# Kernel optimization log

Measured on AMD Instinct MI355X. Metric: run time of the kernel, lower is better.

## Reference

```python
import math
import jax, jax.numpy as jnp
import numpy as np

THETA_RES = 1.0
RHO_RES = 1.0


def _hough_index_table(H, W, theta_res=THETA_RES, rho_res=RHO_RES):
    """Precomputed rho-bin index per (angle, pixel), as in the C_dht CUDA kernel."""
    numangle = int(math.ceil(180.0 / theta_res))
    D = math.sqrt((H - 1) ** 2 + (W - 1) ** 2)
    numrho = int(math.ceil(2.0 * D / rho_res) + 1)
    thetas = np.arange(numangle) * (np.pi / numangle)          # [A]
    xs = (np.arange(W) - W // 2).astype(np.float64)            # centered cols
    ys = (np.arange(H) - H // 2).astype(np.float64)            # centered rows
    # rho[a, y, x] = (x*cos(theta_a) + y*sin(theta_a)) / rho_res
    rho = (xs[None, None, :] * np.cos(thetas)[:, None, None]
           + ys[None, :, None] * np.sin(thetas)[:, None, None]) / rho_res
    ridx = np.round(rho).astype(np.int32) + numrho // 2
    ridx = np.clip(ridx, 0, numrho - 1)
    return jnp.asarray(ridx.reshape(numangle, H * W)), numangle, numrho


def setup_inputs() -> dict:
    key = jax.random.key(0)
    feat = jax.random.normal(key, (4, 128, 256, 256), dtype=jnp.float32)
    return {"feat": feat}


def reference(feat):
    N, C, H, W = feat.shape
    ridx, numangle, numrho = _hough_index_table(H, W)
    # pixels-major layout so segment_sum scatters over the leading axis
    x = feat.reshape(N * C, H * W).T                            # [P, N*C]
    scatter = lambda idx: jax.ops.segment_sum(x, idx, num_segments=numrho)
    acc = jax.vmap(scatter)(ridx)                               # [A, numrho, N*C]
    return acc.transpose(2, 0, 1).reshape(N, C, numangle, numrho)
```

## Files before the change

### kernel.cpp

```cpp
#include <hip/hip_runtime.h>
#include <hip/hip_fp16.h>
#include <cmath>


#define NA 180
#define NR 723
#define HW 65536
#define NC 512
#define ROW_W 368
#define ROW_PAD 368
#define RBASE 176
#define NWIN 32

__device__ __forceinline__ bool is_phase2(int a) { return a >= 46 && a <= 134; }

struct __align__(8) h4 { __half2 a, b; };

__global__ __launch_bounds__(256) void dht_win(unsigned int* __restrict__ win) {
    const int lane = threadIdx.x;
    const int w = blockIdx.x;
    const int a = blockIdx.y;
    const double theta = (double)a * (M_PI / 180.0);
    const double c = cos(theta), s = sin(theta);
    const bool p2 = is_phase2(a);
    int prev = 0;
    unsigned int word = 0;
    #pragma unroll
    for (int i = 0; i < 8; ++i) {
        const int k = w * 8 + i;
        const int x = p2 ? k : lane;
        const int y = p2 ? lane : k;
        const double rho = __dadd_rn(__dmul_rn((double)(x - 128), c),
                                     __dmul_rn((double)(y - 128), s));
        int r = (int)rint(rho) + 361;
        r = min(max(r, 0), NR - 1);
        if (i == 0) word = (unsigned int)r;
        else if (r != prev) word |= (1u << (15 + i));
        prev = r;
    }
    win[((size_t)a * NWIN + w) * 256 + lane] = word;
}

__global__ __launch_bounds__(256) void zero_out(float4* __restrict__ o, int n4) {
    const int i = blockIdx.x * 256 + threadIdx.x;
    if (i < n4) o[i] = make_float4(0.f, 0.f, 0.f, 0.f);
}

template <int SGN>
__device__ __forceinline__ void walk_one(const uint4 wq,
                                         const __half2 (&pxA)[8][4],
                                         const __half2 (&pxB)[8][4],
                                         h4* __restrict__ rp) {
    #pragma unroll
    for (int j = 0; j < 4; ++j) {
        const unsigned int wrd = (&wq.x)[j];
        int bin = (int)(wrd & 0xffffu) - RBASE;
        #pragma unroll
        for (int k = 0; k < 8; ++k) {
            if (k) bin += SGN * (int)((wrd >> (15 + k)) & 1u);
            h4 v = rp[bin];
            v.a = __hadd2(v.a, pxA[k][j]);
            v.b = __hadd2(v.b, pxB[k][j]);
            rp[bin] = v;
        }
    }
}

template <int SGN0, int SGN1>
__device__ __forceinline__ void walk_dual(const uint4 wq0, const uint4 wq1,
                                          const __half2 (&pxA)[8][4],
                                          const __half2 (&pxB)[8][4],
                                          h4* __restrict__ rpA,
                                          h4* __restrict__ rpB) {
    #pragma unroll
    for (int j = 0; j < 4; ++j) {
        const unsigned int w0 = (&wq0.x)[j];
        const unsigned int w1 = (&wq1.x)[j];
        int b0 = (int)(w0 & 0xffffu) - RBASE;
        int b1 = (int)(w1 & 0xffffu) - RBASE;
        #pragma unroll
        for (int k = 0; k < 8; ++k) {
            if (k) {
                b0 += SGN0 * (int)((w0 >> (15 + k)) & 1u);
                b1 += SGN1 * (int)((w1 >> (15 + k)) & 1u);
            }
            h4 vA = rpA[b0];
            h4 vB = rpB[b1];
            vA.a = __hadd2(vA.a, pxA[k][j]);
            vA.b = __hadd2(vA.b, pxB[k][j]);
            vB.a = __hadd2(vB.a, pxA[k][j]);
            vB.b = __hadd2(vB.b, pxB[k][j]);
            rpA[b0] = vA;
            rpB[b1] = vB;
        }
    }
}

__global__ __launch_bounds__(1024, 4) void dht_main(const float* __restrict__ feat,
                                                    const unsigned int* __restrict__ win,
                                                    float* __restrict__ out) {
    __shared__ h4 rowsA[16 * ROW_PAD];
    __shared__ h4 rowsB[16 * ROW_PAD];
    const int t = threadIdx.x;
    const int wv = t >> 6;
    const int l = t & 63;
    const int quad = blockIdx.x;
    const int phase = blockIdx.y;
    const int h = blockIdx.z;
    const int w = 16 * h + wv;
    const int k0 = 8 * w;
    const float* __restrict__ f0 = feat + (size_t)(4 * quad + 0) * HW;
    const float* __restrict__ f1 = feat + (size_t)(4 * quad + 1) * HW;
    const float* __restrict__ f2 = feat + (size_t)(4 * quad + 2) * HW;
    const float* __restrict__ f3 = feat + (size_t)(4 * quad + 3) * HW;
    float* __restrict__ o0 = out + (size_t)(4 * quad + 0) * (NA * NR);
    float* __restrict__ o1 = out + (size_t)(4 * quad + 1) * (NA * NR);
    float* __restrict__ o2 = out + (size_t)(4 * quad + 2) * (NA * NR);
    float* __restrict__ o3 = out + (size_t)(4 * quad + 3) * (NA * NR);

    const int fj0 = 2 * l;
    const int fj2 = 2 * l + 128;

    __half2 pxA[8][4], pxB[8][4];
    if (phase == 0) {
        #pragma unroll
        for (int k = 0; k < 8; ++k) {
            const int ro = (k0 + k) << 8;
            const float2 v0a = *(const float2*)(f0 + ro + fj0);
            const float2 v1a = *(const float2*)(f1 + ro + fj0);
            const float2 v2a = *(const float2*)(f2 + ro + fj0);
            const float2 v3a = *(const float2*)(f3 + ro + fj0);
            const float2 v0b = *(const float2*)(f0 + ro + fj2);
            const float2 v1b = *(const float2*)(f1 + ro + fj2);
            const float2 v2b = *(const float2*)(f2 + ro + fj2);
            const float2 v3b = *(const float2*)(f3 + ro + fj2);
            pxA[k][0] = __floats2half2_rn(v0a.x, v1a.x);
            pxB[k][0] = __floats2half2_rn(v2a.x, v3a.x);
            pxA[k][1] = __floats2half2_rn(v0a.y, v1a.y);
            pxB[k][1] = __floats2half2_rn(v2a.y, v3a.y);
            pxA[k][2] = __floats2half2_rn(v0b.x, v1b.x);
            pxB[k][2] = __floats2half2_rn(v2b.x, v3b.x);
            pxA[k][3] = __floats2half2_rn(v0b.y, v1b.y);
            pxB[k][3] = __floats2half2_rn(v2b.y, v3b.y);
        }
    } else {
        #pragma unroll
        for (int j = 0; j < 4; ++j) {
            const int fr = (j < 2) ? (fj0 + j) : (fj2 + (j - 2));
            const int ro = fr << 8;
            const float4 q0 = *(const float4*)(f0 + ro + k0);
            const float4 q1 = *(const float4*)(f0 + ro + k0 + 4);
            const float4 r0 = *(const float4*)(f1 + ro + k0);
            const float4 r1 = *(const float4*)(f1 + ro + k0 + 4);
            const float4 s0 = *(const float4*)(f2 + ro + k0);
            const float4 s1 = *(const float4*)(f2 + ro + k0 + 4);
            const float4 t0 = *(const float4*)(f3 + ro + k0);
            const float4 t1 = *(const float4*)(f3 + ro + k0 + 4);
            pxA[0][j] = __floats2half2_rn(q0.x, r0.x);
            pxB[0][j] = __floats2half2_rn(s0.x, t0.x);
            pxA[1][j] = __floats2half2_rn(q0.y, r0.y);
            pxB[1][j] = __floats2half2_rn(s0.y, t0.y);
            pxA[2][j] = __floats2half2_rn(q0.z, r0.z);
            pxB[2][j] = __floats2half2_rn(s0.z, t0.z);
            pxA[3][j] = __floats2half2_rn(q0.w, r0.w);
            pxB[3][j] = __floats2half2_rn(s0.w, t0.w);
            pxA[4][j] = __floats2half2_rn(q1.x, r1.x);
            pxB[4][j] = __floats2half2_rn(s1.x, t1.x);
            pxA[5][j] = __floats2half2_rn(q1.y, r1.y);
            pxB[5][j] = __floats2half2_rn(s1.y, t1.y);
            pxA[6][j] = __floats2half2_rn(q1.z, r1.z);
            pxB[6][j] = __floats2half2_rn(s1.z, t1.z);
            pxA[7][j] = __floats2half2_rn(q1.w, r1.w);
            pxB[7][j] = __floats2half2_rn(s1.w, t1.w);
        }
    }

    const int nAng = phase ? 89 : 91;
    for (int cb = 0; cb < nAng; cb += 2) {
        const int cn = min(2, nAng - cb);
        {
            float2* zA = (float2*)rowsA;
            float2* zB = (float2*)rowsB;
            for (int i = t; i < 16 * ROW_PAD; i += 1024) {
                zA[i] = make_float2(0.f, 0.f);
                zB[i] = make_float2(0.f, 0.f);
            }
        }
        __syncthreads();

        const int a0 = phase ? (46 + cb) : (cb <= 45 ? cb : cb + 89);
        h4* __restrict__ rpA = rowsA + wv * ROW_PAD;
        if (cn == 2) {
            const int ax1 = cb + 1;
            const int a1 = phase ? (46 + ax1) : (ax1 <= 45 ? ax1 : ax1 + 89);
            const unsigned int* wr0 = win + ((size_t)a0 * NWIN + w) * 256;
            const unsigned int* wr1 = win + ((size_t)a1 * NWIN + w) * 256;
            const uint2 p00 = *(const uint2*)(wr0 + fj0);
            const uint2 p01 = *(const uint2*)(wr0 + fj2);
            const uint2 p10 = *(const uint2*)(wr1 + fj0);
            const uint2 p11 = *(const uint2*)(wr1 + fj2);
            uint4 wq0; wq0.x = p00.x; wq0.y = p00.y; wq0.z = p01.x; wq0.w = p01.y;
            uint4 wq1; wq1.x = p10.x; wq1.y = p10.y; wq1.z = p11.x; wq1.w = p11.y;
            h4* __restrict__ rpB = rowsB + wv * ROW_PAD;
            if (!phase || a1 <= 90)
                walk_dual<+1, +1>(wq0, wq1, pxA, pxB, rpA, rpB);
            else if (a0 > 90)
                walk_dual<-1, -1>(wq0, wq1, pxA, pxB, rpA, rpB);
            else
                walk_dual<+1, -1>(wq0, wq1, pxA, pxB, rpA, rpB);
        } else {
            const unsigned int* wr0 = win + ((size_t)a0 * NWIN + w) * 256;
            const uint2 p00 = *(const uint2*)(wr0 + fj0);
            const uint2 p01 = *(const uint2*)(wr0 + fj2);
            uint4 wq0; wq0.x = p00.x; wq0.y = p00.y; wq0.z = p01.x; wq0.w = p01.y;
            if (phase && a0 > 90) walk_one<-1>(wq0, pxA, pxB, rpA);
            else                  walk_one<+1>(wq0, pxA, pxB, rpA);
        }
        __syncthreads();

        for (int i = t; i < cn * ROW_W; i += 1024) {
            const int al = i / ROW_W;
            const int rl = i - al * ROW_W;
            const h4* __restrict__ src = al ? rowsB : rowsA;
            float s0 = 0.f, s1 = 0.f, s2 = 0.f, s3 = 0.f;
            #pragma unroll
            for (int c2 = 0; c2 < 16; ++c2) {
                const h4 v = src[c2 * ROW_PAD + rl];
                s0 += __low2float(v.a); s1 += __high2float(v.a);
                s2 += __low2float(v.b); s3 += __high2float(v.b);
            }
            const int aidx = cb + al;
            const int a = phase ? (46 + aidx) : (aidx <= 45 ? aidx : aidx + 89);
            const size_t o = (size_t)a * NR + (RBASE + rl);
            unsafeAtomicAdd(o0 + o, s0);
            unsafeAtomicAdd(o1 + o, s1);
            unsafeAtomicAdd(o2 + o, s2);
            unsafeAtomicAdd(o3 + o, s3);
        }
        __syncthreads();
    }
}

extern "C" void kernel_launch(void* const* d_in, const int* in_sizes, int n_in,
                              void* d_out, int out_size, void* d_ws, size_t ws_size,
                              hipStream_t stream) {
    const float* feat = (const float*)d_in[0];
    float* out = (float*)d_out;
    unsigned int* win = (unsigned int*)d_ws;

    const size_t win_bytes = (size_t)NA * NWIN * 256 * sizeof(unsigned int);
    if (ws_size < win_bytes) return;

    const int n4 = out_size / 4;
    hipLaunchKernelGGL(zero_out, dim3((n4 + 255) / 256), dim3(256), 0, stream,
                       (float4*)out, n4);
    hipLaunchKernelGGL(dht_win, dim3(NWIN, NA), dim3(256), 0, stream, win);
    hipLaunchKernelGGL(dht_main, dim3(NC / 4, 2, 2), dim3(1024), 0, stream,
                       feat, win, out);
}
```

Before: 817.2 us.

## Process eight channels per block with 16-byte LDS bins and 8-wave blocks

Result: slower. 849.9 us (+4.0%).

```diff
diff --git a/kernel.cpp b/kernel.cpp
--- a/kernel.cpp
+++ b/kernel.cpp
@@ -11,10 +11,11 @@
 #define ROW_PAD 368
 #define RBASE 176
 #define NWIN 32
+#define NCP 8
 
 __device__ __forceinline__ bool is_phase2(int a) { return a >= 46 && a <= 134; }
 
-struct __align__(8) h4 { __half2 a, b; };
+struct __align__(16) h8 { __half2 a, b, c, d; };
 
 __global__ __launch_bounds__(256) void dht_win(unsigned int* __restrict__ win) {
     const int lane = threadIdx.x;
@@ -48,9 +49,11 @@
 
 template <int SGN>
 __device__ __forceinline__ void walk_one(const uint4 wq,
-                                         const __half2 (&pxA)[8][4],
-                                         const __half2 (&pxB)[8][4],
-                                         h4* __restrict__ rp) {
+                                         const __half2 (&pP)[8][4],
+                                         const __half2 (&pQ)[8][4],
+                                         const __half2 (&pR)[8][4],
+                                         const __half2 (&pS)[8][4],
+                                         h8* __restrict__ rp) {
     #pragma unroll
     for (int j = 0; j < 4; ++j) {
         const unsigned int wrd = (&wq.x)[j];
@@ -58,9 +61,11 @@
         #pragma unroll
         for (int k = 0; k < 8; ++k) {
             if (k) bin += SGN * (int)((wrd >> (15 + k)) & 1u);
-            h4 v = rp[bin];
-            v.a = __hadd2(v.a, pxA[k][j]);
-            v.b = __hadd2(v.b, pxB[k][j]);
+            h8 v = rp[bin];
+            v.a = __hadd2(v.a, pP[k][j]);
+            v.b = __hadd2(v.b, pQ[k][j]);
+            v.c = __hadd2(v.c, pR[k][j]);
+            v.d = __hadd2(v.d, pS[k][j]);
             rp[bin] = v;
         }
     }
@@ -68,10 +73,12 @@
 
 template <int SGN0, int SGN1>
 __device__ __forceinline__ void walk_dual(const uint4 wq0, const uint4 wq1,
-                                          const __half2 (&pxA)[8][4],
-                                          const __half2 (&pxB)[8][4],
-                                          h4* __restrict__ rpA,
-                                          h4* __restrict__ rpB) {
+                                          const __half2 (&pP)[8][4],
+                                          const __half2 (&pQ)[8][4],
+                                          const __half2 (&pR)[8][4],
+                                          const __half2 (&pS)[8][4],
+                                          h8* __restrict__ rpA,
+                                          h8* __restrict__ rpB) {
     #pragma unroll
     for (int j = 0; j < 4; ++j) {
         const unsigned int w0 = (&wq0.x)[j];
@@ -84,94 +91,111 @@
                 b0 += SGN0 * (int)((w0 >> (15 + k)) & 1u);
                 b1 += SGN1 * (int)((w1 >> (15 + k)) & 1u);
             }
-            h4 vA = rpA[b0];
-            h4 vB = rpB[b1];
-            vA.a = __hadd2(vA.a, pxA[k][j]);
-            vA.b = __hadd2(vA.b, pxB[k][j]);
-            vB.a = __hadd2(vB.a, pxA[k][j]);
-            vB.b = __hadd2(vB.b, pxB[k][j]);
+            h8 vA = rpA[b0];
+            h8 vB = rpB[b1];
+            vA.a = __hadd2(vA.a, pP[k][j]);
+            vA.b = __hadd2(vA.b, pQ[k][j]);
+            vA.c = __hadd2(vA.c, pR[k][j]);
+            vA.d = __hadd2(vA.d, pS[k][j]);
+            vB.a = __hadd2(vB.a, pP[k][j]);
+            vB.b = __hadd2(vB.b, pQ[k][j]);
+            vB.c = __hadd2(vB.c, pR[k][j]);
+            vB.d = __hadd2(vB.d, pS[k][j]);
             rpA[b0] = vA;
             rpB[b1] = vB;
         }
     }
 }
 
-__global__ __launch_bounds__(1024, 4) void dht_main(const float* __restrict__ feat,
-                                                    const unsigned int* __restrict__ win,
-                                                    float* __restrict__ out) {
-    __shared__ h4 rowsA[16 * ROW_PAD];
-    __shared__ h4 rowsB[16 * ROW_PAD];
+__global__ __launch_bounds__(512, 2) void dht_main(const float* __restrict__ feat,
+                                                   const unsigned int* __restrict__ win,
+                                                   float* __restrict__ out) {
+    __shared__ h8 rowsA[NCP * ROW_PAD];
+    __shared__ h8 rowsB[NCP * ROW_PAD];
     const int t = threadIdx.x;
     const int wv = t >> 6;
     const int l = t & 63;
-    const int quad = blockIdx.x;
+    const int oct = blockIdx.x;
     const int phase = blockIdx.y;
-    const int h = blockIdx.z;
-    const int w = 16 * h + wv;
+    const int z = blockIdx.z;
+    const int w = 8 * z + wv;
     const int k0 = 8 * w;
-    const float* __restrict__ f0 = feat + (size_t)(4 * quad + 0) * HW;
-    const float* __restrict__ f1 = feat + (size_t)(4 * quad + 1) * HW;
-    const float* __restrict__ f2 = feat + (size_t)(4 * quad + 2) * HW;
-    const float* __restrict__ f3 = feat + (size_t)(4 * quad + 3) * HW;
-    float* __restrict__ o0 = out + (size_t)(4 * quad + 0) * (NA * NR);
-    float* __restrict__ o1 = out + (size_t)(4 * quad + 1) * (NA * NR);
-    float* __restrict__ o2 = out + (size_t)(4 * quad + 2) * (NA * NR);
-    float* __restrict__ o3 = out + (size_t)(4 * quad + 3) * (NA * NR);
+
+    const float* const fp[8] = {
+        feat + (size_t)(8 * oct + 0) * HW, feat + (size_t)(8 * oct + 1) * HW,
+        feat + (size_t)(8 * oct + 2) * HW, feat + (size_t)(8 * oct + 3) * HW,
+        feat + (size_t)(8 * oct + 4) * HW, feat + (size_t)(8 * oct + 5) * HW,
+        feat + (size_t)(8 * oct + 6) * HW, feat + (size_t)(8 * oct + 7) * HW };
+    float* const op[8] = {
+        out + (size_t)(8 * oct + 0) * (NA * NR), out + (size_t)(8 * oct + 1) * (NA * NR),
+        out + (size_t)(8 * oct + 2) * (NA * NR), out + (size_t)(8 * oct + 3) * (NA * NR),
+        out + (size_t)(8 * oct + 4) * (NA * NR), out + (size_t)(8 * oct + 5) * (NA * NR),
+        out + (size_t)(8 * oct + 6) * (NA * NR), out + (size_t)(8 * oct + 7) * (NA * NR) };
 
     const int fj0 = 2 * l;
     const int fj2 = 2 * l + 128;
 
-    __half2 pxA[8][4], pxB[8][4];
+    __half2 pP[8][4], pQ[8][4], pR[8][4], pS[8][4];
     if (phase == 0) {
         #pragma unroll
         for (int k = 0; k < 8; ++k) {
             const int ro = (k0 + k) << 8;
-            const float2 v0a = *(const float2*)(f0 + ro + fj0);
-            const float2 v1a = *(const float2*)(f1 + ro + fj0);
-            const float2 v2a = *(const float2*)(f2 + ro + fj0);
-            const float2 v3a = *(const float2*)(f3 + ro + fj0);
-            const float2 v0b = *(const float2*)(f0 + ro + fj2);
-            const float2 v1b = *(const float2*)(f1 + ro + fj2);
-            const float2 v2b = *(const float2*)(f2 + ro + fj2);
-            const float2 v3b = *(const float2*)(f3 + ro + fj2);
-            pxA[k][0] = __floats2half2_rn(v0a.x, v1a.x);
-            pxB[k][0] = __floats2half2_rn(v2a.x, v3a.x);
-            pxA[k][1] = __floats2half2_rn(v0a.y, v1a.y);
-            pxB[k][1] = __floats2half2_rn(v2a.y, v3a.y);
-            pxA[k][2] = __floats2half2_rn(v0b.x, v1b.x);
-            pxB[k][2] = __floats2half2_rn(v2b.x, v3b.x);
-            pxA[k][3] = __floats2half2_rn(v0b.y, v1b.y);
-            pxB[k][3] = __floats2half2_rn(v2b.y, v3b.y);
+            float2 u0[8], u2[8];
+            #pragma unroll
+            for (int im = 0; im < 8; ++im) {
+                u0[im] = *(const float2*)(fp[im] + ro + fj0);
+                u2[im] = *(const float2*)(fp[im] + ro + fj2);
+            }
+            pP[k][0] = __floats2half2_rn(u0[0].x, u0[1].x);
+            pQ[k][0] = __floats2half2_rn(u0[2].x, u0[3].x);
+            pR[k][0] = __floats2half2_rn(u0[4].x, u0[5].x);
+            pS[k][0] = __floats2half2_rn(u0[6].x, u0[7].x);
+            pP[k][1] = __floats2half2_rn(u0[0].y, u0[1].y);
+            pQ[k][1] = __floats2half2_rn(u0[2].y, u0[3].y);
+            pR[k][1] = __floats2half2_rn(u0[4].y, u0[5].y);
+            pS[k][1] = __floats2half2_rn(u0[6].y, u0[7].y);
+            pP[k][2] = __floats2half2_rn(u2[0].x, u2[1].x);
+            pQ[k][2] = __floats2half2_rn(u2[2].x, u2[3].x);
+            pR[k][2] = __floats2half2_rn(u2[4].x, u2[5].x);
+            pS[k][2] = __floats2half2_rn(u2[6].x, u2[7].x);
+            pP[k][3] = __floats2half2_rn(u2[0].y, u2[1].y);
+            pQ[k][3] = __floats2half2_rn(u2[2].y, u2[3].y);
+            pR[k][3] = __floats2half2_rn(u2[4].y, u2[5].y);
+            pS[k][3] = __floats2half2_rn(u2[6].y, u2[7].y);
         }
     } else {
         #pragma unroll
         for (int j = 0; j < 4; ++j) {
             const int fr = (j < 2) ? (fj0 + j) : (fj2 + (j - 2));
             const int ro = fr << 8;
-            const float4 q0 = *(const float4*)(f0 + ro + k0);
-            const float4 q1 = *(const float4*)(f0 + ro + k0 + 4);
-            const float4 r0 = *(const float4*)(f1 + ro + k0);
-            const float4 r1 = *(const float4*)(f1 + ro + k0 + 4);
-            const float4 s0 = *(const float4*)(f2 + ro + k0);
-            const float4 s1 = *(const float4*)(f2 + ro + k0 + 4);
-            const float4 t0 = *(const float4*)(f3 + ro + k0);
-            const float4 t1 = *(const float4*)(f3 + ro + k0 + 4);
-            pxA[0][j] = __floats2half2_rn(q0.x, r0.x);
-            pxB[0][j] = __floats2half2_rn(s0.x, t0.x);
-            pxA[1][j] = __floats2half2_rn(q0.y, r0.y);
-            pxB[1][j] = __floats2half2_rn(s0.y, t0.y);
-            pxA[2][j] = __floats2half2_rn(q0.z, r0.z);
-            pxB[2][j] = __floats2half2_rn(s0.z, t0.z);
-            pxA[3][j] = __floats2half2_rn(q0.w, r0.w);
-            pxB[3][j] = __floats2half2_rn(s0.w, t0.w);
-            pxA[4][j] = __floats2half2_rn(q1.x, r1.x);
-            pxB[4][j] = __floats2half2_rn(s1.x, t1.x);
-            pxA[5][j] = __floats2half2_rn(q1.y, r1.y);
-            pxB[5][j] = __floats2half2_rn(s1.y, t1.y);
-            pxA[6][j] = __floats2half2_rn(q1.z, r1.z);
-            pxB[6][j] = __floats2half2_rn(s1.z, t1.z);
-            pxA[7][j] = __floats2half2_rn(q1.w, r1.w);
-            pxB[7][j] = __floats2half2_rn(s1.w, t1.w);
+            float4 qa[8], qb[8];
+            #pragma unroll
+            for (int im = 0; im < 8; ++im) {
+                qa[im] = *(const float4*)(fp[im] + ro + k0);
+                qb[im] = *(const float4*)(fp[im] + ro + k0 + 4);
+            }
+            #pragma unroll
+            for (int k = 0; k < 4; ++k) {
+                const float v0 = (&qa[0].x)[k], v1 = (&qa[1].x)[k];
+                const float v2 = (&qa[2].x)[k], v3 = (&qa[3].x)[k];
+                const float v4 = (&qa[4].x)[k], v5 = (&qa[5].x)[k];
+                const float v6 = (&qa[6].x)[k], v7 = (&qa[7].x)[k];
+                pP[k][j] = __floats2half2_rn(v0, v1);
+                pQ[k][j] = __floats2half2_rn(v2, v3);
+                pR[k][j] = __floats2half2_rn(v4, v5);
+                pS[k][j] = __floats2half2_rn(v6, v7);
+            }
+            #pragma unroll
+            for (int k = 0; k < 4; ++k) {
+                const float v0 = (&qb[0].x)[k], v1 = (&qb[1].x)[k];
+                const float v2 = (&qb[2].x)[k], v3 = (&qb[3].x)[k];
+                const float v4 = (&qb[4].x)[k], v5 = (&qb[5].x)[k];
+                const float v6 = (&qb[6].x)[k], v7 = (&qb[7].x)[k];
+                pP[k + 4][j] = __floats2half2_rn(v0, v1);
+                pQ[k + 4][j] = __floats2half2_rn(v2, v3);
+                pR[k + 4][j] = __floats2half2_rn(v4, v5);
+                pS[k + 4][j] = __floats2half2_rn(v6, v7);
+            }
         }
     }
 
@@ -179,17 +203,17 @@
     for (int cb = 0; cb < nAng; cb += 2) {
         const int cn = min(2, nAng - cb);
         {
-            float2* zA = (float2*)rowsA;
-            float2* zB = (float2*)rowsB;
-            for (int i = t; i < 16 * ROW_PAD; i += 1024) {
-                zA[i] = make_float2(0.f, 0.f);
-                zB[i] = make_float2(0.f, 0.f);
+            float4* zA = (float4*)rowsA;
+            float4* zB = (float4*)rowsB;
+            for (int i = t; i < NCP * ROW_PAD; i += 512) {
+                zA[i] = make_float4(0.f, 0.f, 0.f, 0.f);
+                zB[i] = make_float4(0.f, 0.f, 0.f, 0.f);
             }
         }
         __syncthreads();
 
         const int a0 = phase ? (46 + cb) : (cb <= 45 ? cb : cb + 89);
-        h4* __restrict__ rpA = rowsA + wv * ROW_PAD;
+        h8* __restrict__ rpA = rowsA + wv * ROW_PAD;
         if (cn == 2) {
             const int ax1 = cb + 1;
             const int a1 = phase ? (46 + ax1) : (ax1 <= 45 ? ax1 : ax1 + 89);
@@ -201,41 +225,48 @@
             const uint2 p11 = *(const uint2*)(wr1 + fj2);
             uint4 wq0; wq0.x = p00.x; wq0.y = p00.y; wq0.z = p01.x; wq0.w = p01.y;
             uint4 wq1; wq1.x = p10.x; wq1.y = p10.y; wq1.z = p11.x; wq1.w = p11.y;
-            h4* __restrict__ rpB = rowsB + wv * ROW_PAD;
+            h8* __restrict__ rpB = rowsB + wv * ROW_PAD;
             if (!phase || a1 <= 90)
-                walk_dual<+1, +1>(wq0, wq1, pxA, pxB, rpA, rpB);
+                walk_dual<+1, +1>(wq0, wq1, pP, pQ, pR, pS, rpA, rpB);
             else if (a0 > 90)
-                walk_dual<-1, -1>(wq0, wq1, pxA, pxB, rpA, rpB);
+                walk_dual<-1, -1>(wq0, wq1, pP, pQ, pR, pS, rpA, rpB);
             else
-                walk_dual<+1, -1>(wq0, wq1, pxA, pxB, rpA, rpB);
+                walk_dual<+1, -1>(wq0, wq1, pP, pQ, pR, pS, rpA, rpB);
         } else {
             const unsigned int* wr0 = win + ((size_t)a0 * NWIN + w) * 256;
             const uint2 p00 = *(const uint2*)(wr0 + fj0);
             const uint2 p01 = *(const uint2*)(wr0 + fj2);
             uint4 wq0; wq0.x = p00.x; wq0.y = p00.y; wq0.z = p01.x; wq0.w = p01.y;
-            if (phase && a0 > 90) walk_one<-1>(wq0, pxA, pxB, rpA);
-            else                  walk_one<+1>(wq0, pxA, pxB, rpA);
+            if (phase && a0 > 90) walk_one<-1>(wq0, pP, pQ, pR, pS, rpA);
+            else                  walk_one<+1>(wq0, pP, pQ, pR, pS, rpA);
         }
         __syncthreads();
 
-        for (int i = t; i < cn * ROW_W; i += 1024) {
+        for (int i = t; i < cn * ROW_W; i += 512) {
             const int al = i / ROW_W;
             const int rl = i - al * ROW_W;
-            const h4* __restrict__ src = al ? rowsB : rowsA;
+            const h8* __restrict__ src = al ? rowsB : rowsA;
             float s0 = 0.f, s1 = 0.f, s2 = 0.f, s3 = 0.f;
-            #pragma unroll
-            for (int c2 = 0; c2 < 16; ++c2) {
-                const h4 v = src[c2 * ROW_PAD + rl];
+            float s4 = 0.f, s5 = 0.f, s6 = 0.f, s7 = 0.f;
+            #pragma unroll
+            for (int c2 = 0; c2 < NCP; ++c2) {
+                const h8 v = src[c2 * ROW_PAD + rl];
                 s0 += __low2float(v.a); s1 += __high2float(v.a);
                 s2 += __low2float(v.b); s3 += __high2float(v.b);
+                s4 += __low2float(v.c); s5 += __high2float(v.c);
+                s6 += __low2float(v.d); s7 += __high2float(v.d);
             }
             const int aidx = cb + al;
             const int a = phase ? (46 + aidx) : (aidx <= 45 ? aidx : aidx + 89);
             const size_t o = (size_t)a * NR + (RBASE + rl);
-            unsafeAtomicAdd(o0 + o, s0);
-            unsafeAtomicAdd(o1 + o, s1);
-            unsafeAtomicAdd(o2 + o, s2);
-            unsafeAtomicAdd(o3 + o, s3);
+            unsafeAtomicAdd(op[0] + o, s0);
+            unsafeAtomicAdd(op[1] + o, s1);
+            unsafeAtomicAdd(op[2] + o, s2);
+            unsafeAtomicAdd(op[3] + o, s3);
+            unsafeAtomicAdd(op[4] + o, s4);
+            unsafeAtomicAdd(op[5] + o, s5);
+            unsafeAtomicAdd(op[6] + o, s6);
+            unsafeAtomicAdd(op[7] + o, s7);
         }
         __syncthreads();
     }
@@ -255,6 +286,6 @@
     hipLaunchKernelGGL(zero_out, dim3((n4 + 255) / 256), dim3(256), 0, stream,
                        (float4*)out, n4);
     hipLaunchKernelGGL(dht_win, dim3(NWIN, NA), dim3(256), 0, stream, win);
-    hipLaunchKernelGGL(dht_main, dim3(NC / 4, 2, 2), dim3(1024), 0, stream,
+    hipLaunchKernelGGL(dht_main, dim3(NC / 8, 2, 4), dim3(512), 0, stream,
                        feat, win, out);
 }
```
